# Performance work log

Measured on AMD Instinct MI355X. Metric: run time of the kernel, lower is better.

## Reference

```python
import jax, jax.numpy as jnp
import numpy as np

TOP_K = 2  # matches init k


def setup_inputs() -> dict:
    key = jax.random.key(0)
    ks = jax.random.split(key, 5)
    B, S, D, E, H = 2, 2048, 1024, 8, 4096
    scale = 0.02
    return {
        "x": jax.random.normal(ks[0], (B, S, D), dtype=jnp.float32),
        "wg": jax.random.normal(ks[1], (D, E), dtype=jnp.float32) * scale,
        "w1": jax.random.normal(ks[2], (E, D, H), dtype=jnp.float32) * scale,
        "w3": jax.random.normal(ks[3], (E, D, H), dtype=jnp.float32) * scale,
        "w2": jax.random.normal(ks[4], (E, H, D), dtype=jnp.float32) * scale,
    }


def reference(x, wg, w1, w3, w2):
    # x: [B, S, D]; wg: [D, E]; w1/w3: [E, D, H]; w2: [E, H, D]
    B, S, D = x.shape
    E = wg.shape[1]
    T = B * S
    xt = x.reshape(T, D)

    # Top-k gating: softmax over expert logits, keep top-k, renormalize.
    logits = xt @ wg                                    # [T, E]
    probs = jax.nn.softmax(logits, axis=-1)             # [T, E]
    topv, topi = jax.lax.top_k(probs, TOP_K)            # [T, k]
    topv = topv / topv.sum(axis=-1, keepdims=True)
    # Dense combine weights [T, E] (zero for non-selected experts).
    comb = jnp.zeros((T, E), dtype=x.dtype).at[jnp.arange(T)[:, None], topi].set(topv)

    # Per-expert SwiGLU MLP with weighted combine (loop over small fixed E).
    out = jnp.zeros_like(xt)
    for e in range(E):
        h = jax.nn.silu(xt @ w1[e]) * (xt @ w3[e])      # [T, H]
        out = out + comb[:, e:e + 1] * (h @ w2[e])       # [T, D]
    return out.reshape(B, S, D)
```

## Files before the change

kernel.cpp:

```cpp
#include <hip/hip_runtime.h>
#include <cstdint>
#include <cstddef>

#define T_TOK 4096
#define DIM   1024
#define NEXP  8
#define HDIM  4096
#define NSLOT (2 * T_TOK)

#define BM 128
#define BN1 128
#define BN2 256
#define BK 32

typedef __attribute__((ext_vector_type(8))) short s16x8;
typedef __attribute__((ext_vector_type(4))) float f32x4;

__device__ __forceinline__ unsigned short f2bf(float f) {
    union { float f; unsigned u; } v; v.f = f;
    unsigned u = v.u;
    unsigned r = (u + 0x7FFFu + ((u >> 16) & 1u)) >> 16;
    return (unsigned short)r;
}

__device__ __forceinline__ int lds_off(int row, int kchunk) {
    return row * 32 + ((kchunk ^ ((row >> 1) & 3)) << 3);
}

__device__ __forceinline__ void gload16(const void* g, void* l) {
    __builtin_amdgcn_global_load_lds(
        (const __attribute__((address_space(1))) unsigned int*)g,
        (__attribute__((address_space(3))) unsigned int*)l, 16, 0, 0);
}

__global__ __launch_bounds__(256) void gate_kernel(
    const float* __restrict__ x, const float* __restrict__ wg,
    int* __restrict__ tok_e, float* __restrict__ tok_w, int* __restrict__ counts,
    unsigned short* __restrict__ xg)
{
    int t = blockIdx.x * 4 + (threadIdx.x >> 6);
    int lane = threadIdx.x & 63;
    float acc[NEXP];
#pragma unroll
    for (int e = 0; e < NEXP; ++e) acc[e] = 0.f;
    const float* xrow = x + (size_t)t * DIM;
    unsigned short* xgrow = xg + (size_t)t * DIM;
    for (int d = lane; d < DIM; d += 64) {
        float xv = xrow[d];
        xgrow[d] = f2bf(xv);
        const float4* wr = (const float4*)(wg + (size_t)d * NEXP);
        float4 w0 = wr[0], w1v = wr[1];
        acc[0] += xv * w0.x;  acc[1] += xv * w0.y;
        acc[2] += xv * w0.z;  acc[3] += xv * w0.w;
        acc[4] += xv * w1v.x; acc[5] += xv * w1v.y;
        acc[6] += xv * w1v.z; acc[7] += xv * w1v.w;
    }
#pragma unroll
    for (int e = 0; e < NEXP; ++e)
#pragma unroll
        for (int off = 32; off > 0; off >>= 1)
            acc[e] += __shfl_xor(acc[e], off);
    if (lane == 0) {
        int i0 = 0;
#pragma unroll
        for (int e = 1; e < NEXP; ++e) if (acc[e] > acc[i0]) i0 = e;
        int i1 = (i0 == 0) ? 1 : 0;
#pragma unroll
        for (int e = 0; e < NEXP; ++e) if (e != i0 && acc[e] > acc[i1]) i1 = e;
        float w0 = 1.f / (1.f + __expf(acc[i1] - acc[i0]));
        tok_e[2 * t] = i0;  tok_e[2 * t + 1] = i1;
        tok_w[2 * t] = w0;  tok_w[2 * t + 1] = 1.f - w0;
        atomicAdd(&counts[i0], 1);
        atomicAdd(&counts[i1], 1);
    }
}

__global__ void scan_kernel(const int* __restrict__ counts,
                            int* __restrict__ offsets, int* __restrict__ cursor)
{
    if (threadIdx.x == 0) {
        int s = 0;
        for (int e = 0; e < NEXP; ++e) { offsets[e] = s; s += counts[e]; cursor[e] = 0; }
        offsets[NEXP] = s;
    }
}

__global__ __launch_bounds__(256) void assign_kernel(
    const int* __restrict__ tok_e, const float* __restrict__ tok_w,
    const int* __restrict__ offsets, int* __restrict__ cursor,
    int* __restrict__ rows_tok, float* __restrict__ rows_gate)
{
    int t = blockIdx.x * 256 + threadIdx.x;
    if (t >= T_TOK) return;
#pragma unroll
    for (int j = 0; j < 2; ++j) {
        int e = tok_e[2 * t + j];
        int pos = offsets[e] + atomicAdd(&cursor[e], 1);
        rows_tok[pos] = t;
        rows_gate[pos] = tok_w[2 * t + j];
    }
}

__device__ __forceinline__ void tconv_body(
    const float* __restrict__ src, unsigned short* __restrict__ dst,
    int R, int C, int e, int bx, int by, int t)
{
    __shared__ unsigned int t_lds[64 * 33];
    int c0 = bx * 64, r0 = by * 64;
    int lane = t & 63, w = t >> 6;
    const float* s = src + (size_t)e * R * C + (size_t)(r0 + w * 16) * C + c0 + lane;
#pragma unroll
    for (int j = 0; j < 8; ++j) {
        float v0 = s[(size_t)(2 * j) * C];
        float v1 = s[(size_t)(2 * j + 1) * C];
        unsigned int pk = (unsigned int)f2bf(v0) | ((unsigned int)f2bf(v1) << 16);
        t_lds[lane * 33 + (w * 8 + j)] = pk;
    }
    __syncthreads();
    unsigned short* dbase = dst + (size_t)e * C * R;
#pragma unroll
    for (int rep = 0; rep < 2; ++rep) {
        int idx = rep * 256 + t;
        int c = idx >> 3, chunk = idx & 7;
        uint4 o;
        o.x = t_lds[c * 33 + chunk * 4 + 0];
        o.y = t_lds[c * 33 + chunk * 4 + 1];
        o.z = t_lds[c * 33 + chunk * 4 + 2];
        o.w = t_lds[c * 33 + chunk * 4 + 3];
        *(uint4*)(dbase + (size_t)(c0 + c) * R + r0 + chunk * 8) = o;
    }
}

__global__ __launch_bounds__(256) void tconv13_kernel(
    const float* __restrict__ w1, const float* __restrict__ w3,
    unsigned short* __restrict__ w1t, unsigned short* __restrict__ w3t)
{
    int z = blockIdx.z;
    if (z < NEXP)
        tconv_body(w1, w1t, DIM, HDIM, z, blockIdx.x, blockIdx.y, threadIdx.x);
    else
        tconv_body(w3, w3t, DIM, HDIM, z - NEXP, blockIdx.x, blockIdx.y, threadIdx.x);
}

__global__ __launch_bounds__(256) void tconv_kernel(
    const float* __restrict__ src, unsigned short* __restrict__ dst, int R, int C)
{
    tconv_body(src, dst, R, C, blockIdx.z, blockIdx.x, blockIdx.y, threadIdx.x);
}

__global__ __launch_bounds__(512, 4) void gemm1_kernel(
    const unsigned short* __restrict__ xg,
    const unsigned short* __restrict__ w1t, const unsigned short* __restrict__ w3t,
    const int* __restrict__ rows_tok, const int* __restrict__ offsets,
    unsigned short* __restrict__ h)
{
    int e = blockIdx.z;
    int offs = offsets[e];
    int cnt  = offsets[e + 1] - offs;
    int m0 = blockIdx.y * BM;
    if (m0 >= cnt) return;
    int n0 = blockIdx.x * BN1;

    __shared__ unsigned short As[2][BM * BK];
    __shared__ unsigned short B1s[2][BN1 * BK];
    __shared__ unsigned short B3s[2][BN1 * BK];
    __shared__ int toks[BM];

    int tid = threadIdx.x;
    if (tid < BM) toks[tid] = rows_tok[offs + min(m0 + tid, cnt - 1)];
    __syncthreads();

    int lane = tid & 63;
    int wid = tid >> 6;
    int wr = wid >> 2, wc = wid & 3;
    int lr = lane & 15, lg = lane >> 4;

    int srow = tid >> 2;
    int g = (tid & 3) ^ ((srow >> 1) & 3);
    const unsigned short* asrc  = xg  + (size_t)toks[srow] * DIM + g * 8;
    const unsigned short* b1src = w1t + ((size_t)e * HDIM + n0 + srow) * DIM + g * 8;
    const unsigned short* b3src = w3t + ((size_t)e * HDIM + n0 + srow) * DIM + g * 8;
    int ldsbase = wid * 512;

    f32x4 acc1[4][2] = {};
    f32x4 acc3[4][2] = {};

    auto stage = [&](int buf, int k0) {
        gload16(asrc + k0,  &As[buf][ldsbase]);
        gload16(b1src + k0, &B1s[buf][ldsbase]);
        gload16(b3src + k0, &B3s[buf][ldsbase]);
    };

    auto compute = [&](int buf) {
        s16x8 a[4];
#pragma unroll
        for (int m = 0; m < 4; ++m)
            a[m] = *(const s16x8*)&As[buf][lds_off(wr * 64 + m * 16 + lr, lg)];
#pragma unroll
        for (int n = 0; n < 2; ++n) {
            int rowb = wc * 32 + n * 16 + lr;
            s16x8 b1f = *(const s16x8*)&B1s[buf][lds_off(rowb, lg)];
            s16x8 b3f = *(const s16x8*)&B3s[buf][lds_off(rowb, lg)];
#pragma unroll
            for (int m = 0; m < 4; ++m)
                acc1[m][n] = __builtin_amdgcn_mfma_f32_16x16x32_bf16(a[m], b1f, acc1[m][n], 0, 0, 0);
#pragma unroll
            for (int m = 0; m < 4; ++m)
                acc3[m][n] = __builtin_amdgcn_mfma_f32_16x16x32_bf16(a[m], b3f, acc3[m][n], 0, 0, 0);
        }
    };

    stage(0, 0);
    __syncthreads();
    int buf = 0;
    for (int kt = 1; kt < DIM / BK; ++kt) {
        stage(buf ^ 1, kt * BK);
        compute(buf);
        __syncthreads();
        buf ^= 1;
    }
    compute(buf);

#pragma unroll
    for (int m = 0; m < 4; ++m)
#pragma unroll
        for (int n = 0; n < 2; ++n)
#pragma unroll
            for (int r = 0; r < 4; ++r) {
                int row_local = wr * 64 + m * 16 + lg * 4 + r;
                if (m0 + row_local < cnt) {
                    int col_local = wc * 32 + n * 16 + lr;
                    float g1 = acc1[m][n][r];
                    float hv = (g1 / (1.f + __expf(-g1))) * acc3[m][n][r];
                    h[(size_t)(offs + m0 + row_local) * HDIM + n0 + col_local] = f2bf(hv);
                }
            }
}

__global__ __launch_bounds__(512, 4) void gemm2_kernel(
    const unsigned short* __restrict__ h, const unsigned short* __restrict__ w2t,
    const int* __restrict__ rows_tok, const float* __restrict__ rows_gate,
    const int* __restrict__ offsets, float* __restrict__ out)
{
    int e = blockIdx.z;
    int offs = offsets[e];
    int cnt  = offsets[e + 1] - offs;
    int m0 = blockIdx.y * BM;
    if (m0 >= cnt) return;
    int n0 = blockIdx.x * BN2;

    __shared__ unsigned short As[2][BM * BK];
    __shared__ unsigned short Bs[2][BN2 * BK];
    __shared__ int   toks[BM];
    __shared__ float gts[BM];

    int tid = threadIdx.x;
    if (tid < BM) {
        int p = offs + min(m0 + tid, cnt - 1);
        toks[tid] = rows_tok[p];
        gts[tid]  = rows_gate[p];
    }

    int lane = tid & 63;
    int wid = tid >> 6;
    int wr = wid >> 2, wc = wid & 3;
    int lr = lane & 15, lg = lane >> 4;

    int srow = tid >> 2;
    int g = (tid & 3) ^ ((srow >> 1) & 3);
    int arow = offs + min(m0 + srow, cnt - 1);
    const unsigned short* asrc = h + (size_t)arow * HDIM + g * 8;
    const unsigned short* bsrc0 = w2t + ((size_t)e * DIM + n0 + srow) * HDIM + g * 8;
    const unsigned short* bsrc1 = w2t + ((size_t)e * DIM + n0 + 128 + srow) * HDIM + g * 8;
    int ldsA = wid * 512;

    f32x4 acc[4][4] = {};

    auto stage = [&](int buf, int k0) {
        gload16(asrc + k0,  &As[buf][ldsA]);
        gload16(bsrc0 + k0, &Bs[buf][ldsA]);
        gload16(bsrc1 + k0, &Bs[buf][4096 + ldsA]);
    };

    auto compute = [&](int buf) {
        s16x8 a[4];
#pragma unroll
        for (int m = 0; m < 4; ++m)
            a[m] = *(const s16x8*)&As[buf][lds_off(wr * 64 + m * 16 + lr, lg)];
#pragma unroll
        for (int n = 0; n < 4; ++n) {
            s16x8 bf = *(const s16x8*)&Bs[buf][lds_off(wc * 64 + n * 16 + lr, lg)];
#pragma unroll
            for (int m = 0; m < 4; ++m)
                acc[m][n] = __builtin_amdgcn_mfma_f32_16x16x32_bf16(a[m], bf, acc[m][n], 0, 0, 0);
        }
    };

    __syncthreads();
    stage(0, 0);
    __syncthreads();
    int buf = 0;
    for (int kt = 1; kt < HDIM / BK; ++kt) {
        stage(buf ^ 1, kt * BK);
        compute(buf);
        __syncthreads();
        buf ^= 1;
    }
    compute(buf);

#pragma unroll
    for (int m = 0; m < 4; ++m)
#pragma unroll
        for (int n = 0; n < 4; ++n)
#pragma unroll
            for (int r = 0; r < 4; ++r) {
                int row_local = wr * 64 + m * 16 + lg * 4 + r;
                if (m0 + row_local < cnt) {
                    int col = n0 + wc * 64 + n * 16 + lr;
                    float v = acc[m][n][r] * gts[row_local];
                    atomicAdd(&out[(size_t)toks[row_local] * DIM + col], v);
                }
            }
}

extern "C" void kernel_launch(void* const* d_in, const int* in_sizes, int n_in,
                              void* d_out, int out_size, void* d_ws, size_t ws_size,
                              hipStream_t stream)
{
    const float* x  = (const float*)d_in[0];
    const float* wg = (const float*)d_in[1];
    const float* w1 = (const float*)d_in[2];
    const float* w3 = (const float*)d_in[3];
    const float* w2 = (const float*)d_in[4];
    float* out = (float*)d_out;

    char* ws = (char*)d_ws;
    size_t off = 0;
    auto alloc = [&](size_t bytes) -> void* {
        void* p = ws + off;
        off = (off + bytes + 255) & ~(size_t)255;
        return p;
    };
    int*   rows_tok  = (int*)alloc((size_t)NSLOT * 4);
    float* rows_gate = (float*)alloc((size_t)NSLOT * 4);
    int*   tok_e     = (int*)alloc((size_t)NSLOT * 4);
    float* tok_w     = (float*)alloc((size_t)NSLOT * 4);
    int*   counts    = (int*)alloc(NEXP * 4);
    int*   offsets   = (int*)alloc((NEXP + 1) * 4);
    int*   cursor    = (int*)alloc(NEXP * 4);
    unsigned short* xg   = (unsigned short*)alloc((size_t)T_TOK * DIM * 2);
    unsigned short* w1t  = (unsigned short*)alloc((size_t)NEXP * HDIM * DIM * 2);
    unsigned short* w3t  = (unsigned short*)alloc((size_t)NEXP * HDIM * DIM * 2);
    unsigned short* hbuf = (unsigned short*)alloc((size_t)NSLOT * HDIM * 2);
    unsigned short* w2t  = w1t;

    hipMemsetAsync(counts, 0, NEXP * 4, stream);
    hipMemsetAsync(out, 0, (size_t)out_size * sizeof(float), stream);

    gate_kernel<<<T_TOK / 4, 256, 0, stream>>>(x, wg, tok_e, tok_w, counts, xg);
    scan_kernel<<<1, 64, 0, stream>>>(counts, offsets, cursor);
    assign_kernel<<<T_TOK / 256, 256, 0, stream>>>(tok_e, tok_w, offsets, cursor,
                                                   rows_tok, rows_gate);

    tconv13_kernel<<<dim3(HDIM / 64, DIM / 64, 2 * NEXP), 256, 0, stream>>>(
        w1, w3, w1t, w3t);

    gemm1_kernel<<<dim3(HDIM / BN1, T_TOK / BM, NEXP), 512, 0, stream>>>(
        xg, w1t, w3t, rows_tok, offsets, hbuf);

    tconv_kernel<<<dim3(DIM / 64, HDIM / 64, NEXP), 256, 0, stream>>>(w2, w2t, HDIM, DIM);

    gemm2_kernel<<<dim3(DIM / BN2, T_TOK / BM, NEXP), 512, 0, stream>>>(
        hbuf, w2t, rows_tok, rows_gate, offsets, out);
}
```

Measured before the change: 580.8 us.

## Triple-buffer gemm1 LDS with BK=64 and explicit waitcnt/barrier scheduling

Replaces the double-buffered BK=32 pipeline in the fused w1/w3 GEMM with a three-stage LDS ring of 64-wide K tiles, each split into two 32-wide sub-stages. Loads are issued two tiles ahead and synchronised with explicit vmcnt/lgkmcnt waits, raw s_barrier calls and sched_barrier, and the MFMA block is wrapped in s_setprio to favour math issue. The larger LDS footprint (about 144 KB) forces launch bounds down to 2 blocks per CU, trading occupancy for deeper prefetch and fewer sync points per K step.

```diff
diff --git a/kernel.cpp b/kernel.cpp
--- a/kernel.cpp
+++ b/kernel.cpp
@@ -148,7 +148,7 @@
     tconv_body(src, dst, R, C, blockIdx.z, blockIdx.x, blockIdx.y, threadIdx.x);
 }
 
-__global__ __launch_bounds__(512, 4) void gemm1_kernel(
+__global__ __launch_bounds__(512, 2) void gemm1_kernel(
     const unsigned short* __restrict__ xg,
     const unsigned short* __restrict__ w1t, const unsigned short* __restrict__ w3t,
     const int* __restrict__ rows_tok, const int* __restrict__ offsets,
@@ -161,9 +161,7 @@
     if (m0 >= cnt) return;
     int n0 = blockIdx.x * BN1;
 
-    __shared__ unsigned short As[2][BM * BK];
-    __shared__ unsigned short B1s[2][BN1 * BK];
-    __shared__ unsigned short B3s[2][BN1 * BK];
+    __shared__ unsigned short lds3[3][3][8192];
     __shared__ int toks[BM];
 
     int tid = threadIdx.x;
@@ -185,41 +183,60 @@
     f32x4 acc1[4][2] = {};
     f32x4 acc3[4][2] = {};
 
-    auto stage = [&](int buf, int k0) {
-        gload16(asrc + k0,  &As[buf][ldsbase]);
-        gload16(b1src + k0, &B1s[buf][ldsbase]);
-        gload16(b3src + k0, &B3s[buf][ldsbase]);
+    const int NT = DIM / 64;
+
+    auto stage_sub = [&](int b, int t, int s) {
+        int k0 = t * 64 + s * 32;
+        int db = s * 4096 + ldsbase;
+        gload16(asrc + k0,  &lds3[b][0][db]);
+        gload16(b1src + k0, &lds3[b][1][db]);
+        gload16(b3src + k0, &lds3[b][2][db]);
     };
 
-    auto compute = [&](int buf) {
-        s16x8 a[4];
-#pragma unroll
-        for (int m = 0; m < 4; ++m)
-            a[m] = *(const s16x8*)&As[buf][lds_off(wr * 64 + m * 16 + lr, lg)];
-#pragma unroll
-        for (int n = 0; n < 2; ++n) {
-            int rowb = wc * 32 + n * 16 + lr;
-            s16x8 b1f = *(const s16x8*)&B1s[buf][lds_off(rowb, lg)];
-            s16x8 b3f = *(const s16x8*)&B3s[buf][lds_off(rowb, lg)];
+    stage_sub(0, 0, 0); stage_sub(0, 0, 1);
+    stage_sub(1, 1, 0); stage_sub(1, 1, 1);
+
+    int cur = 0;
+    for (int t = 0; t < NT; ++t) {
+        if (t == NT - 1) asm volatile("s_waitcnt vmcnt(0)" ::: "memory");
+        else             asm volatile("s_waitcnt vmcnt(6)" ::: "memory");
+        __builtin_amdgcn_sched_barrier(0);
+        __builtin_amdgcn_s_barrier();
+
+        int nxt = cur + 2; if (nxt >= 3) nxt -= 3;
+#pragma unroll
+        for (int s = 0; s < 2; ++s) {
+            int sub = s * 4096;
+            s16x8 a[4], b1f[2], b3f[2];
 #pragma unroll
             for (int m = 0; m < 4; ++m)
-                acc1[m][n] = __builtin_amdgcn_mfma_f32_16x16x32_bf16(a[m], b1f, acc1[m][n], 0, 0, 0);
-#pragma unroll
-            for (int m = 0; m < 4; ++m)
-                acc3[m][n] = __builtin_amdgcn_mfma_f32_16x16x32_bf16(a[m], b3f, acc3[m][n], 0, 0, 0);
+                a[m] = *(const s16x8*)&lds3[cur][0][sub + lds_off(wr * 64 + m * 16 + lr, lg)];
+#pragma unroll
+            for (int n = 0; n < 2; ++n) {
+                b1f[n] = *(const s16x8*)&lds3[cur][1][sub + lds_off(wc * 32 + n * 16 + lr, lg)];
+                b3f[n] = *(const s16x8*)&lds3[cur][2][sub + lds_off(wc * 32 + n * 16 + lr, lg)];
+            }
+            if (t + 2 < NT) stage_sub(nxt, t + 2, s);
+
+            __builtin_amdgcn_s_barrier();
+            asm volatile("s_waitcnt lgkmcnt(0)" ::: "memory");
+            __builtin_amdgcn_sched_barrier(0);
+
+            __builtin_amdgcn_s_setprio(1);
+#pragma unroll
+            for (int n = 0; n < 2; ++n) {
+#pragma unroll
+                for (int m = 0; m < 4; ++m)
+                    acc1[m][n] = __builtin_amdgcn_mfma_f32_16x16x32_bf16(a[m], b1f[n], acc1[m][n], 0, 0, 0);
+#pragma unroll
+                for (int m = 0; m < 4; ++m)
+                    acc3[m][n] = __builtin_amdgcn_mfma_f32_16x16x32_bf16(a[m], b3f[n], acc3[m][n], 0, 0, 0);
+            }
+            __builtin_amdgcn_s_setprio(0);
+            if (s == 0) __builtin_amdgcn_s_barrier();
         }
-    };
-
-    stage(0, 0);
-    __syncthreads();
-    int buf = 0;
-    for (int kt = 1; kt < DIM / BK; ++kt) {
-        stage(buf ^ 1, kt * BK);
-        compute(buf);
-        __syncthreads();
-        buf ^= 1;
-    }
-    compute(buf);
+        cur = cur + 1; if (cur == 3) cur = 0;
+    }
 
 #pragma unroll
     for (int m = 0; m < 4; ++m)
```

After: 641.0 us. 10.4% more time.
